# Performance work log

Hardware: AMD Instinct MI355X
Metric: run time of the kernel (lower is better)

## Reference

```python
import jax, jax.numpy as jnp
import numpy as np

D_MODEL = 1024
N_HEADS = 16
N_GROUPS = 4
D_K = D_MODEL // N_HEADS
HEADS_PER_GROUP = N_HEADS // N_GROUPS


def rope(x):
    # x: [b, s, d]; rotate using half-split concat (NOT interleaved), matching source
    s, d = x.shape[1], x.shape[2]
    theta = 1.0 / (10000.0 ** (jnp.arange(d // 2, dtype=jnp.float32) / (d // 2)))
    ang = jnp.arange(s, dtype=jnp.float32)[:, None] * theta[None, :]  # [s, d/2]
    cos, sin = jnp.cos(ang), jnp.sin(ang)
    xe, xo = x[..., 0::2], x[..., 1::2]
    return jnp.concatenate([xe * cos - xo * sin, xe * sin + xo * cos], axis=-1)


def setup_inputs() -> dict:
    key = jax.random.key(0)
    k1, k2, k3, k4, k5 = jax.random.split(key, 5)
    b, s = 1, 2048
    scale = 0.02
    X = jax.random.normal(k1, (b, s, D_MODEL), dtype=jnp.float32)
    W_q = jax.random.normal(k2, (D_MODEL, D_MODEL), dtype=jnp.float32) * scale
    W_k = jax.random.normal(k3, (N_GROUPS * D_K, D_MODEL), dtype=jnp.float32) * scale
    W_v = jax.random.normal(k4, (N_GROUPS * D_K, D_MODEL), dtype=jnp.float32) * scale
    W_o = jax.random.normal(k5, (D_MODEL, D_MODEL), dtype=jnp.float32) * scale
    return {"X": X, "W_q": W_q, "W_k": W_k, "W_v": W_v, "W_o": W_o}


def reference(X, W_q, W_k, W_v, W_o):
    b, s, _ = X.shape
    Xr = rope(X)
    Q = (Xr @ W_q.T).reshape(b, s, N_HEADS, D_K).transpose(0, 2, 1, 3)
    K = (Xr @ W_k.T).reshape(b, s, N_GROUPS, D_K).transpose(0, 2, 1, 3)
    V = (Xr @ W_v.T).reshape(b, s, N_GROUPS, D_K).transpose(0, 2, 1, 3)
    Q = Q.reshape(b, N_GROUPS, HEADS_PER_GROUP, s, D_K)
    scores = jnp.einsum('bghsd,bgtd->bghst', Q, K) / jnp.sqrt(jnp.float32(D_K))
    mask = jnp.triu(jnp.ones((s, s), dtype=scores.dtype), k=1) * (-1e9)
    attn = jax.nn.softmax(scores + mask, axis=-1)
    out = jnp.einsum('bghst,bgtd->bghsd', attn, V)  # [b,g,h,s,dk]
    out = out.reshape(b, N_HEADS, s, D_K).transpose(0, 2, 1, 3).reshape(b, s, D_MODEL)
    return out @ W_o.T
```

## Files before the change

kernel.cpp:

```cpp
#include <hip/hip_runtime.h>
#include <hip/hip_bf16.h>

#define S_LEN   2048
#define D_MODEL 1024
#define N_HEADS 16
#define N_GROUPS 4
#define D_K     64
#define KV_DIM  (N_GROUPS * D_K)

typedef __hip_bfloat16 bf16;
typedef unsigned short u16;
typedef __attribute__((ext_vector_type(8))) short bfrag;
typedef __attribute__((ext_vector_type(4))) float ffrag;
typedef __attribute__((ext_vector_type(4))) unsigned int u32x4;

__device__ __forceinline__ float b2f(u16 u) {
    return __uint_as_float(((unsigned)u) << 16);
}
__device__ __forceinline__ u16 f2bu(float f) {
    bf16 h = __float2bfloat16(f);
    return __builtin_bit_cast(u16, h);
}
__device__ __forceinline__ unsigned cvt_pk_bf16(float lo, float hi) {
    unsigned r;
    asm("v_cvt_pk_bf16_f32 %0, %1, %2" : "=v"(r) : "v"(lo), "v"(hi));
    return r;
}
__device__ __forceinline__ float ex2(float x) {
#if __has_builtin(__builtin_amdgcn_exp2f)
    return __builtin_amdgcn_exp2f(x);
#else
    return __expf(x * 0.69314718f);
#endif
}

typedef __attribute__((address_space(3))) u16 lds_u16;
typedef __attribute__((address_space(1))) const u16 glb_u16;
__device__ __forceinline__ void gld_lds16(const u16* g, u16* l) {
    __builtin_amdgcn_global_load_lds((glb_u16*)g, (lds_u16*)l, 16, 0, 0);
}

__device__ __forceinline__ int probe_f32(const u16* p) {
    int lane = threadIdx.x & 63;
    int e0 = (p[lane] >> 7) & 0xFF;
    int e1 = (p[lane + 64] >> 7) & 0xFF;
    int c = ((e0 < 100 || e0 > 140) ? 1 : 0) + ((e1 < 100 || e1 > 140) ? 1 : 0);
    unsigned long long b1 = __ballot(c >= 1);
    unsigned long long b2 = __ballot(c >= 2);
    return ((__popcll(b1) + __popcll(b2)) > 16) ? 1 : 0;
}

__global__ void probe5_kernel(const u16* __restrict__ p0, const u16* __restrict__ p1,
                              const u16* __restrict__ p2, const u16* __restrict__ p3,
                              const u16* __restrict__ p4, int* __restrict__ mode) {
    if (blockIdx.x != 0) return;
    const u16* ps[5] = {p0, p1, p2, p3, p4};
    int lane = threadIdx.x & 63;
    for (int t = 0; t < 5; t++) {
        int e0 = (ps[t][lane] >> 7) & 0xFF;
        int e1 = (ps[t][lane + 64] >> 7) & 0xFF;
        int c = ((e0 < 100 || e0 > 140) ? 1 : 0) + ((e1 < 100 || e1 > 140) ? 1 : 0);
        unsigned long long b1 = __ballot(c >= 1);
        unsigned long long b2 = __ballot(c >= 2);
        if (lane == 0) mode[t] = ((__popcll(b1) + __popcll(b2)) > 16) ? 1 : 0;
    }
}

__global__ __launch_bounds__(512)
void rope_kernel(const void* __restrict__ Xin, u16* __restrict__ Xr) {
    int md = probe_f32((const u16*)Xin);
    int i = blockIdx.x;
    int j = threadIdx.x;
    float freq = ex2(-(float)j * 0.025952563241307518f);
    float ang  = (float)i * freq;
    float sv, cv;
    sincosf(ang, &sv, &cv);
    int base = i * D_MODEL;
    float xe, xo;
    if (md) {
        float2 xv = *(const float2*)&((const float*)Xin)[base + 2 * j];
        xe = xv.x; xo = xv.y;
    } else {
        ushort2 xv = *(const ushort2*)&((const u16*)Xin)[base + 2 * j];
        xe = b2f(xv.x); xo = b2f(xv.y);
    }
    Xr[base + j]       = f2bu(xe * cv - xo * sv);
    Xr[base + 512 + j] = f2bu(xe * sv + xo * cv);
}

__global__ __launch_bounds__(256)
void wconv_kernel(const void* __restrict__ Wq, const void* __restrict__ Wk,
                  const void* __restrict__ Wv, const void* __restrict__ Wo,
                  u16* __restrict__ WB, u16* __restrict__ WoB) {
    int bid = blockIdx.x;
    const void* src; u16* dst; int gbase;
    if (bid < 512)      { src = Wq; dst = WB;                      gbase = bid; }
    else if (bid < 640) { src = Wk; dst = WB + 1024 * 1024;        gbase = bid - 512; }
    else if (bid < 768) { src = Wv; dst = WB + 1280 * 1024;        gbase = bid - 640; }
    else                { src = Wo; dst = WoB;                     gbase = bid - 768; }
    int md = probe_f32((const u16*)src);
    size_t g = (size_t)gbase * 256 + threadIdx.x;
    if (md) {
        const float* f = (const float*)src + g * 8;
        float4 v0 = *(const float4*)f;
        float4 v1 = *(const float4*)(f + 4);
        u16 t[8] = {f2bu(v0.x), f2bu(v0.y), f2bu(v0.z), f2bu(v0.w),
                    f2bu(v1.x), f2bu(v1.y), f2bu(v1.z), f2bu(v1.w)};
        *(uint4*)(dst + g * 8) = *(const uint4*)t;
    } else {
        *(uint4*)(dst + g * 8) = *(const uint4*)((const u16*)src + g * 8);
    }
}

template<int MODE>
__global__ __launch_bounds__(256)
void gemm_fast(const u16* __restrict__ A, const u16* __restrict__ WBm,
               u16* __restrict__ Qm, u16* __restrict__ Km, u16* __restrict__ Vm,
               float* __restrict__ Cf) {
    __shared__ u16 As[8192];
    __shared__ u16 Bs[4096];
    const int tid = threadIdx.x;
    const int w = tid >> 6, lane = tid & 63, quad = lane >> 4, lcol = lane & 15;
    const int m0 = blockIdx.y * 128;
    const int n0 = blockIdx.x * 64;

    const int arl   = lane >> 3;
    const int colsw = ((lane & 7) ^ arl) * 8;

    const u16* ap[4]; const u16* bp[2];
    u16* asd[4]; u16* bsd[2];
    #pragma unroll
    for (int c = 0; c < 4; c++) {
        ap[c]  = A + (size_t)(m0 + (c * 4 + w) * 8 + arl) * 1024 + colsw;
        asd[c] = As + (c * 4 + w) * 512;
    }
    #pragma unroll
    for (int c = 0; c < 2; c++) {
        bp[c]  = WBm + (size_t)(n0 + (c * 4 + w) * 8 + arl) * 1024 + colsw;
        bsd[c] = Bs + (c * 4 + w) * 512;
    }

    const int abase = (w * 32 + lcol) * 64;
    const int koff0 = (quad * 8) ^ ((lcol & 7) * 8);
    const int koff1 = koff0 ^ 32;

    ffrag acc[2][4];
    #pragma unroll
    for (int rf = 0; rf < 2; rf++)
        #pragma unroll
        for (int ct = 0; ct < 4; ct++) acc[rf][ct] = (ffrag)0.0f;

    for (int k0 = 0; k0 < D_MODEL; k0 += 64) {
        #pragma unroll
        for (int c = 0; c < 4; c++) gld_lds16(ap[c] + k0, asd[c]);
        #pragma unroll
        for (int c = 0; c < 2; c++) gld_lds16(bp[c] + k0, bsd[c]);
        __syncthreads();

        const bfrag a00 = *(const bfrag*)&As[abase + koff0];
        const bfrag a10 = *(const bfrag*)&As[abase + 1024 + koff0];
        const bfrag a01 = *(const bfrag*)&As[abase + koff1];
        const bfrag a11 = *(const bfrag*)&As[abase + 1024 + koff1];
        #pragma unroll
        for (int ct = 0; ct < 4; ct++) {
            const int bb = (ct * 16 + lcol) * 64;
            const bfrag b0 = *(const bfrag*)&Bs[bb + koff0];
            acc[0][ct] = __builtin_amdgcn_mfma_f32_16x16x32_bf16(a00, b0, acc[0][ct], 0, 0, 0);
            acc[1][ct] = __builtin_amdgcn_mfma_f32_16x16x32_bf16(a10, b0, acc[1][ct], 0, 0, 0);
            const bfrag b1 = *(const bfrag*)&Bs[bb + koff1];
            acc[0][ct] = __builtin_amdgcn_mfma_f32_16x16x32_bf16(a01, b1, acc[0][ct], 0, 0, 0);
            acc[1][ct] = __builtin_amdgcn_mfma_f32_16x16x32_bf16(a11, b1, acc[1][ct], 0, 0, 0);
        }
        __syncthreads();
    }

    if (MODE == 0) {
        if (n0 < 1280) {
            u16* Cp; int ldc, nc;
            if (n0 < 1024) { Cp = Qm; ldc = 1024; nc = n0; }
            else           { Cp = Km; ldc = 256;  nc = n0 - 1024; }
            #pragma unroll
            for (int rf = 0; rf < 2; rf++)
                #pragma unroll
                for (int ct = 0; ct < 4; ct++)
                    #pragma unroll
                    for (int r = 0; r < 4; r++) {
                        int row = m0 + w * 32 + rf * 16 + quad * 4 + r;
                        Cp[(size_t)row * ldc + nc + ct * 16 + lcol] = f2bu(acc[rf][ct][r]);
                    }
        } else {
            const int nc = n0 - 1280;
            #pragma unroll
            for (int rf = 0; rf < 2; rf++)
                #pragma unroll
                for (int ct = 0; ct < 4; ct++)
                    #pragma unroll
                    for (int r = 0; r < 4; r++) {
                        int row = m0 + w * 32 + rf * 16 + quad * 4 + r;
                        int col = nc + ct * 16 + lcol;
                        Vm[(size_t)col * S_LEN + row] = f2bu(acc[rf][ct][r]);
                    }
        }
    } else {
        #pragma unroll
        for (int rf = 0; rf < 2; rf++)
            #pragma unroll
            for (int ct = 0; ct < 4; ct++)
                #pragma unroll
                for (int r = 0; r < 4; r++) {
                    int row = m0 + w * 32 + rf * 16 + quad * 4 + r;
                    Cf[(size_t)row * D_MODEL + n0 + ct * 16 + lcol] = acc[rf][ct][r];
                }
    }
}

__device__ __forceinline__ void stageB(u16* dst, const void* Bv, size_t off, int md) {
    if (md) {
        const float* Bf = (const float*)Bv;
        float4 b0 = *(const float4*)&Bf[off];
        float4 b1 = *(const float4*)&Bf[off + 4];
        u16 t[8] = {f2bu(b0.x), f2bu(b0.y), f2bu(b0.z), f2bu(b0.w),
                    f2bu(b1.x), f2bu(b1.y), f2bu(b1.z), f2bu(b1.w)};
        *(uint4*)dst = *(const uint4*)t;
    } else {
        *(uint4*)dst = *(const uint4*)&((const u16*)Bv)[off];
    }
}

__global__ __launch_bounds__(256)
void qkv_mfma(const u16* __restrict__ Xr, const void* __restrict__ Wq,
              const void* __restrict__ Wk, const void* __restrict__ Wv,
              u16* __restrict__ Qm, u16* __restrict__ Km, u16* __restrict__ Vm,
              const int* __restrict__ mode) {
    __shared__ u16 As[128][36];
    __shared__ u16 Bs[64][36];
    const int tid = threadIdx.x;
    const int w = tid >> 6, lane = tid & 63, quad = lane >> 4, lcol = lane & 15;
    const int m0 = blockIdx.y * 128;
    const int n0 = blockIdx.x * 64;

    const void* Bv; int nb, md;
    if (n0 < 1024)       { Bv = Wq; nb = n0;        md = mode[1]; }
    else if (n0 < 1280)  { Bv = Wk; nb = n0 - 1024; md = mode[2]; }
    else                 { Bv = Wv; nb = n0 - 1280; md = mode[3]; }

    ffrag acc[2][4];
    #pragma unroll
    for (int rf = 0; rf < 2; rf++)
        #pragma unroll
        for (int ct = 0; ct < 4; ct++) acc[rf][ct] = (ffrag)0.0f;

    const int arow = tid >> 2, akc = tid & 3;
    for (int k0 = 0; k0 < D_MODEL; k0 += 32) {
        *(uint4*)&As[arow][akc * 8] =
            *(const uint4*)&Xr[(size_t)(m0 + arow) * D_MODEL + k0 + akc * 8];
        *(uint4*)&As[arow + 64][akc * 8] =
            *(const uint4*)&Xr[(size_t)(m0 + arow + 64) * D_MODEL + k0 + akc * 8];
        stageB(&Bs[arow][akc * 8], Bv, (size_t)(nb + arow) * D_MODEL + k0 + akc * 8, md);
        __syncthreads();
        const bfrag a0 = *(const bfrag*)&As[w * 32 + lcol][quad * 8];
        const bfrag a1 = *(const bfrag*)&As[w * 32 + 16 + lcol][quad * 8];
        #pragma unroll
        for (int ct = 0; ct < 4; ct++) {
            const bfrag b = *(const bfrag*)&Bs[ct * 16 + lcol][quad * 8];
            acc[0][ct] = __builtin_amdgcn_mfma_f32_16x16x32_bf16(a0, b, acc[0][ct], 0, 0, 0);
            acc[1][ct] = __builtin_amdgcn_mfma_f32_16x16x32_bf16(a1, b, acc[1][ct], 0, 0, 0);
        }
        __syncthreads();
    }

    if (n0 < 1280) {
        u16* Cp; int ldc, nc;
        if (n0 < 1024) { Cp = Qm; ldc = 1024; nc = n0; }
        else           { Cp = Km; ldc = 256;  nc = n0 - 1024; }
        #pragma unroll
        for (int rf = 0; rf < 2; rf++)
            #pragma unroll
            for (int ct = 0; ct < 4; ct++)
                #pragma unroll
                for (int r = 0; r < 4; r++) {
                    int row = m0 + w * 32 + rf * 16 + quad * 4 + r;
                    Cp[(size_t)row * ldc + nc + ct * 16 + lcol] = f2bu(acc[rf][ct][r]);
                }
    } else {
        const int nc = n0 - 1280;
        #pragma unroll
        for (int rf = 0; rf < 2; rf++)
            #pragma unroll
            for (int ct = 0; ct < 4; ct++)
                #pragma unroll
                for (int r = 0; r < 4; r++) {
                    int row = m0 + w * 32 + rf * 16 + quad * 4 + r;
                    int col = nc + ct * 16 + lcol;
                    Vm[(size_t)col * S_LEN + row] = f2bu(acc[rf][ct][r]);
                }
    }
}

__global__ __launch_bounds__(256)
void oproj_mfma(const u16* __restrict__ A, const void* __restrict__ B,
                float* __restrict__ C, const int* __restrict__ mode) {
    __shared__ u16 As[128][36];
    __shared__ u16 Bs[64][36];
    const int tid = threadIdx.x;
    const int w = tid >> 6, lane = tid & 63, quad = lane >> 4, lcol = lane & 15;
    const int m0 = blockIdx.y * 128;
    const int n0 = blockIdx.x * 64;
    const int md = mode[4];

    ffrag acc[2][4];
    #pragma unroll
    for (int rf = 0; rf < 2; rf++)
        #pragma unroll
        for (int ct = 0; ct < 4; ct++) acc[rf][ct] = (ffrag)0.0f;

    const int arow = tid >> 2, akc = tid & 3;
    for (int k0 = 0; k0 < D_MODEL; k0 += 32) {
        *(uint4*)&As[arow][akc * 8] =
            *(const uint4*)&A[(size_t)(m0 + arow) * D_MODEL + k0 + akc * 8];
        *(uint4*)&As[arow + 64][akc * 8] =
            *(const uint4*)&A[(size_t)(m0 + arow + 64) * D_MODEL + k0 + akc * 8];
        stageB(&Bs[arow][akc * 8], B, (size_t)(n0 + arow) * D_MODEL + k0 + akc * 8, md);
        __syncthreads();
        const bfrag a0 = *(const bfrag*)&As[w * 32 + lcol][quad * 8];
        const bfrag a1 = *(const bfrag*)&As[w * 32 + 16 + lcol][quad * 8];
        #pragma unroll
        for (int ct = 0; ct < 4; ct++) {
            const bfrag b = *(const bfrag*)&Bs[ct * 16 + lcol][quad * 8];
            acc[0][ct] = __builtin_amdgcn_mfma_f32_16x16x32_bf16(a0, b, acc[0][ct], 0, 0, 0);
            acc[1][ct] = __builtin_amdgcn_mfma_f32_16x16x32_bf16(a1, b, acc[1][ct], 0, 0, 0);
        }
        __syncthreads();
    }

    #pragma unroll
    for (int rf = 0; rf < 2; rf++)
        #pragma unroll
        for (int ct = 0; ct < 4; ct++)
            #pragma unroll
            for (int r = 0; r < 4; r++) {
                int row = m0 + w * 32 + rf * 16 + quad * 4 + r;
                C[(size_t)row * D_MODEL + n0 + ct * 16 + lcol] = acc[rf][ct][r];
            }
}

template<int CS, int SF>
__global__ __launch_bounds__(256)
void attn_part(const u16* __restrict__ Q, const u16* __restrict__ K,
               const u16* __restrict__ Vt, float* __restrict__ OpF,
               u16* __restrict__ OpH, float2* __restrict__ ml2) {
    const int bid = blockIdx.x;
    const int cidx = bid >> 4;
    const int h = bid & 15;
    const int g = h >> 2;

    int i, c;
    if (CS == 3) {
        if (cidx < 8)       { i = cidx;                  c = 0; }
        else if (cidx < 24) { i = 8 + ((cidx - 8) >> 1); c = (cidx - 8) & 1; }
        else if (cidx < 48) { int q = (cidx - 24) / 3;   i = 16 + q; c = (cidx - 24) - 3 * q; }
        else                { i = 24 + ((cidx - 48) >> 2); c = (cidx - 48) & 3; }
    } else {
        if (cidx < 16) { i = cidx; c = 0; }
        else           { i = 16 + ((cidx - 16) >> 1); c = (cidx - 16) & 1; }
    }
    const int i0 = i * 64;
    const int tile0 = c << CS;
    const int tlast = min(i, ((c + 1) << CS) - 1);
    const int nt = tlast - tile0 + 1;

    const int tid  = threadIdx.x;
    const int w    = tid >> 6;
    const int lane = tid & 63;
    const int quad = lane >> 4;
    const int lcol = lane & 15;

    __shared__ u16 Ks[64][72];
    __shared__ u16 Vts[64][72];

    const int qi = i0 + w * 16 + lcol;
    const bfrag qb0 = *(const bfrag*)&Q[(size_t)qi * D_MODEL + h * 64 + quad * 8];
    const bfrag qb1 = *(const bfrag*)&Q[(size_t)qi * D_MODEL + h * 64 + 32 + quad * 8];

    ffrag oacc[4];
    #pragma unroll
    for (int ct = 0; ct < 4; ct++) oacc[ct] = (ffrag)0.0f;
    float m_run = -1e30f, l_run = 0.0f;

    const int key0 = tid & 63, dc0 = tid >> 6;
    const int vd0 = tid >> 3, vch = tid & 7;
    const int vpos0 = 32 * (vch >> 2) + 16 * (vch & 1) + 4 * ((vch >> 1) & 1);
    const u16* vbase0 = &Vt[(size_t)(g * 64 + vd0) * S_LEN];
    const u16* vbase1 = &Vt[(size_t)(g * 64 + vd0 + 32) * S_LEN];

    int jp = tile0 * 64;
    uint4 kpre0 = *(const uint4*)&K[(size_t)(jp + key0) * KV_DIM + g * 64 + dc0 * 8];
    uint4 kpre1 = *(const uint4*)&K[(size_t)(jp + key0) * KV_DIM + g * 64 + (dc0 + 4) * 8];
    uint4 vpre0 = *(const uint4*)&vbase0[jp + vch * 8];
    uint4 vpre1 = *(const uint4*)&vbase1[jp + vch * 8];

    const float CF = 0.18033688f;

    for (int tt = 0; tt < nt; tt++) {
        const int j0 = (tile0 + tt) * 64;

        *(uint4*)&Ks[key0][dc0 * 8]       = kpre0;
        *(uint4*)&Ks[key0][(dc0 + 4) * 8] = kpre1;
        *(uint2*)&Vts[vd0][vpos0]           = make_uint2(vpre0.x, vpre0.y);
        *(uint2*)&Vts[vd0][vpos0 + 8]       = make_uint2(vpre0.z, vpre0.w);
        *(uint2*)&Vts[vd0 + 32][vpos0]      = make_uint2(vpre1.x, vpre1.y);
        *(uint2*)&Vts[vd0 + 32][vpos0 + 8]  = make_uint2(vpre1.z, vpre1.w);
        __syncthreads();

        if (tt + 1 < nt) {
            const int j0n = (tile0 + tt + 1) * 64;
            kpre0 = *(const uint4*)&K[(size_t)(j0n + key0) * KV_DIM + g * 64 + dc0 * 8];
            kpre1 = *(const uint4*)&K[(size_t)(j0n + key0) * KV_DIM + g * 64 + (dc0 + 4) * 8];
            vpre0 = *(const uint4*)&vbase0[j0n + vch * 8];
            vpre1 = *(const uint4*)&vbase1[j0n + vch * 8];
        }

        ffrag sacc[4];
        #pragma unroll
        for (int ct = 0; ct < 4; ct++) sacc[ct] = (ffrag)0.0f;
        __builtin_amdgcn_s_setprio(1);
        #pragma unroll
        for (int ct = 0; ct < 4; ct++) {
            const bfrag kb0 = *(const bfrag*)&Ks[ct * 16 + lcol][quad * 8];
            sacc[ct] = __builtin_amdgcn_mfma_f32_16x16x32_bf16(kb0, qb0, sacc[ct], 0, 0, 0);
            const bfrag kb1 = *(const bfrag*)&Ks[ct * 16 + lcol][32 + quad * 8];
            sacc[ct] = __builtin_amdgcn_mfma_f32_16x16x32_bf16(kb1, qb1, sacc[ct], 0, 0, 0);
        }
        __builtin_amdgcn_s_setprio(0);

        float sv[4][4];
        if (tile0 + tt == i) {
            #pragma unroll
            for (int ct = 0; ct < 4; ct++)
                #pragma unroll
                for (int r = 0; r < 4; r++) {
                    int kj = j0 + ct * 16 + quad * 4 + r;
                    sv[ct][r] = (kj <= qi) ? sacc[ct][r] : -1e30f;
                }
        } else {
            #pragma unroll
            for (int ct = 0; ct < 4; ct++)
                #pragma unroll
                for (int r = 0; r < 4; r++) sv[ct][r] = sacc[ct][r];
        }

        float mx = sv[0][0];
        #pragma unroll
        for (int ct = 0; ct < 4; ct++)
            #pragma unroll
            for (int r = 0; r < 4; r++) mx = fmaxf(mx, sv[ct][r]);
        mx = fmaxf(mx, __shfl_xor(mx, 16, 64));
        mx = fmaxf(mx, __shfl_xor(mx, 32, 64));

        if (!__all(mx <= m_run + 44.0f)) {
            float mnew = fmaxf(m_run, mx);
            float al = ex2((m_run - mnew) * CF);
            m_run = mnew;
            l_run *= al;
            #pragma unroll
            for (int r = 0; r < 4; r++) {
                float ar = __shfl(al, quad * 4 + r, 64);
                #pragma unroll
                for (int ct = 0; ct < 4; ct++) oacc[ct][r] *= ar;
            }
        }

        const float mc = m_run * CF;
        float rs = 0.0f;
        #pragma unroll
        for (int ct = 0; ct < 4; ct++)
            #pragma unroll
            for (int r = 0; r < 4; r++) {
                float p = ex2(sv[ct][r] * CF - mc);
                sv[ct][r] = p;
                rs += p;
            }
        rs += __shfl_xor(rs, 16, 64);
        rs += __shfl_xor(rs, 32, 64);
        l_run += rs;

        u32x4 pw0, pw1;
        pw0[0] = cvt_pk_bf16(sv[0][0], sv[0][1]);
        pw0[1] = cvt_pk_bf16(sv[0][2], sv[0][3]);
        pw0[2] = cvt_pk_bf16(sv[1][0], sv[1][1]);
        pw0[3] = cvt_pk_bf16(sv[1][2], sv[1][3]);
        pw1[0] = cvt_pk_bf16(sv[2][0], sv[2][1]);
        pw1[1] = cvt_pk_bf16(sv[2][2], sv[2][3]);
        pw1[2] = cvt_pk_bf16(sv[3][0], sv[3][1]);
        pw1[3] = cvt_pk_bf16(sv[3][2], sv[3][3]);
        const bfrag pa0 = __builtin_bit_cast(bfrag, pw0);
        const bfrag pa1 = __builtin_bit_cast(bfrag, pw1);

        __builtin_amdgcn_s_setprio(1);
        #pragma unroll
        for (int ct = 0; ct < 4; ct++) {
            const bfrag vb0 = *(const bfrag*)&Vts[ct * 16 + lcol][quad * 8];
            oacc[ct] = __builtin_amdgcn_mfma_f32_16x16x32_bf16(pa0, vb0, oacc[ct], 0, 0, 0);
            const bfrag vb1 = *(const bfrag*)&Vts[ct * 16 + lcol][32 + quad * 8];
            oacc[ct] = __builtin_amdgcn_mfma_f32_16x16x32_bf16(pa1, vb1, oacc[ct], 0, 0, 0);
        }
        __builtin_amdgcn_s_setprio(0);
        __syncthreads();
    }

    #pragma unroll
    for (int ct = 0; ct < 4; ct++)
        #pragma unroll
        for (int r = 0; r < 4; r++) {
            int row = w * 16 + quad * 4 + r;
            size_t off = (size_t)bid * 4096 + row * 64 + ct * 16 + lcol;
            if (SF) OpF[off] = oacc[ct][r];
            else    OpH[off] = f2bu(oacc[ct][r]);
        }
    if (quad == 0)
        ml2[(size_t)bid * 64 + w * 16 + lcol] = make_float2(m_run * 0.125f, l_run);
}

template<int CS, int SF>
__global__ __launch_bounds__(256)
void attn_combine(const float* __restrict__ OpF, const u16* __restrict__ OpH,
                  const float2* __restrict__ ml2, u16* __restrict__ Om) {
    const int row = blockIdx.x;
    const int i = row >> 6;
    const int r = row & 63;
    const int t = threadIdx.x;
    const int h = t >> 4;
    const int d = (t & 15) * 4;
    const int nc = (i >> CS) + 1;
    int pfx;
    if (CS == 3)
        pfx = (i < 8) ? i : (i < 16) ? 8 + 2 * (i - 8)
            : (i < 24) ? 24 + 3 * (i - 16) : 48 + 4 * (i - 24);
    else
        pfx = (i < 16) ? i : 16 + 2 * (i - 16);

    float M = -1e30f;
    for (int c = 0; c < nc; c++) {
        float2 m = ml2[(size_t)((pfx + c) * 16 + h) * 64 + r];
        M = fmaxf(M, m.x);
    }
    float L = 0.0f;
    float acc[4] = {0.0f, 0.0f, 0.0f, 0.0f};
    for (int c = 0; c < nc; c++) {
        float2 m = ml2[(size_t)((pfx + c) * 16 + h) * 64 + r];
        float wgt = __expf(m.x - M);
        L += m.y * wgt;
        size_t off = (size_t)((pfx + c) * 16 + h) * 4096 + r * 64 + d;
        if (SF) {
            float4 v = *(const float4*)&OpF[off];
            acc[0] += v.x * wgt; acc[1] += v.y * wgt;
            acc[2] += v.z * wgt; acc[3] += v.w * wgt;
        } else {
            ushort4 v = *(const ushort4*)&OpH[off];
            acc[0] += b2f(v.x) * wgt; acc[1] += b2f(v.y) * wgt;
            acc[2] += b2f(v.z) * wgt; acc[3] += b2f(v.w) * wgt;
        }
    }
    float inv = 1.0f / L;
    #pragma unroll
    for (int k = 0; k < 4; k++)
        Om[(size_t)row * D_MODEL + h * 64 + d + k] = f2bu(acc[k] * inv);
}

extern "C" void kernel_launch(void* const* d_in, const int* in_sizes, int n_in,
                              void* d_out, int out_size, void* d_ws, size_t ws_size,
                              hipStream_t stream) {
    const void* X  = d_in[0];
    const void* Wq = d_in[1];
    const void* Wk = d_in[2];
    const void* Wv = d_in[3];
    const void* Wo = d_in[4];
    float* out = (float*)d_out;

    u16* XrB = (u16*)d_out;

    int* mode = (int*)d_ws;
    u16* Qm = (u16*)((char*)d_ws + 64);
    u16* Km = Qm + (size_t)S_LEN * D_MODEL;
    u16* Vm = Km + (size_t)S_LEN * KV_DIM;
    u16* Om = Vm + (size_t)S_LEN * KV_DIM;

    const size_t needA    = 10485824ULL + 20971520ULL + 655360ULL;
    const size_t needFull = needA + 3145728ULL + 2097152ULL;

    rope_kernel<<<S_LEN, 512, 0, stream>>>(X, XrB);

    if (ws_size >= needFull) {
        float*  OpF = (float*)((char*)d_ws + 10485824);
        float2* ml2 = (float2*)((char*)d_ws + 10485824 + 20971520);
        u16*    WB  = (u16*)((char*)d_ws + needA);
        u16*    WoB = WB + (size_t)1536 * 1024;

        wconv_kernel<<<1280, 256, 0, stream>>>(Wq, Wk, Wv, Wo, WB, WoB);
        gemm_fast<0><<<dim3(24, 16), 256, 0, stream>>>(XrB, WB, Qm, Km, Vm, nullptr);
        attn_part<3, 1><<<80 * 16, 256, 0, stream>>>(Qm, Km, Vm, OpF, nullptr, ml2);
        attn_combine<3, 1><<<S_LEN, 256, 0, stream>>>(OpF, nullptr, ml2, Om);
        gemm_fast<1><<<dim3(16, 16), 256, 0, stream>>>(Om, WoB, nullptr, nullptr, nullptr, out);
    } else {
        probe5_kernel<<<1, 64, 0, stream>>>(
            (const u16*)X, (const u16*)Wq, (const u16*)Wk, (const u16*)Wv,
            (const u16*)Wo, mode);
        qkv_mfma<<<dim3((D_MODEL + 2 * KV_DIM) / 64, S_LEN / 128), 256, 0, stream>>>(
            XrB, Wq, Wk, Wv, Qm, Km, Vm, mode);
        if (ws_size >= needA) {
            float*  OpF = (float*)((char*)d_ws + 10485824);
            float2* ml2 = (float2*)((char*)d_ws + 10485824 + 20971520);
            attn_part<3, 1><<<80 * 16, 256, 0, stream>>>(Qm, Km, Vm, OpF, nullptr, ml2);
            attn_combine<3, 1><<<S_LEN, 256, 0, stream>>>(OpF, nullptr, ml2, Om);
        } else {
            u16*    OpH = (u16*)d_out;
            float2* ml2 = (float2*)((char*)d_out + (size_t)768 * 4096 * 2);
            attn_part<4, 0><<<48 * 16, 256, 0, stream>>>(Qm, Km, Vm, nullptr, OpH, ml2);
            attn_combine<4, 0><<<S_LEN, 256, 0, stream>>>(nullptr, OpH, ml2, Om);
        }
        oproj_mfma<<<dim3(D_MODEL / 64, S_LEN / 128), 256, 0, stream>>>(Om, Wo, out, mode);
    }
}
```

Before: 144.6 us.

## Double-buffer GEMM and attention LDS tiles, fuse rope and weight conversion

Merges the rope and weight-conversion kernels into a single prep launch, removing one kernel launch. The projection GEMM now double-buffers its LDS tiles, so the next K-slice is loaded while MFMAs run on the current one, dropping one barrier per iteration. The attention kernel likewise double-buffers its K/V tiles and writes the next tile after the PV MFMAs, with one sync per iteration. This doubles LDS use per block, which may reduce occupancy.

Measured after the change: 141.8 us. -2.0%, faster.

```diff
diff --git a/kernel.cpp b/kernel.cpp
--- a/kernel.cpp
+++ b/kernel.cpp
@@ -63,6 +63,53 @@
         unsigned long long b1 = __ballot(c >= 1);
         unsigned long long b2 = __ballot(c >= 2);
         if (lane == 0) mode[t] = ((__popcll(b1) + __popcll(b2)) > 16) ? 1 : 0;
+    }
+}
+
+__global__ __launch_bounds__(512)
+void prep_kernel(const void* __restrict__ Xin, u16* __restrict__ Xr,
+                 const void* __restrict__ Wq, const void* __restrict__ Wk,
+                 const void* __restrict__ Wv, const void* __restrict__ Wo,
+                 u16* __restrict__ WB, u16* __restrict__ WoB) {
+    int b = blockIdx.x;
+    if (b < S_LEN) {
+        int md = probe_f32((const u16*)Xin);
+        int i = b;
+        int j = threadIdx.x;
+        float freq = ex2(-(float)j * 0.025952563241307518f);
+        float ang  = (float)i * freq;
+        float sv, cv;
+        sincosf(ang, &sv, &cv);
+        int base = i * D_MODEL;
+        float xe, xo;
+        if (md) {
+            float2 xv = *(const float2*)&((const float*)Xin)[base + 2 * j];
+            xe = xv.x; xo = xv.y;
+        } else {
+            ushort2 xv = *(const ushort2*)&((const u16*)Xin)[base + 2 * j];
+            xe = b2f(xv.x); xo = b2f(xv.y);
+        }
+        Xr[base + j]       = f2bu(xe * cv - xo * sv);
+        Xr[base + 512 + j] = f2bu(xe * sv + xo * cv);
+    } else {
+        int bid = b - S_LEN;
+        const void* src; u16* dst; int goff;
+        if (bid < 256)      { src = Wq; dst = WB;               goff = bid; }
+        else if (bid < 320) { src = Wk; dst = WB + 1024 * 1024; goff = bid - 256; }
+        else if (bid < 384) { src = Wv; dst = WB + 1280 * 1024; goff = bid - 320; }
+        else                { src = Wo; dst = WoB;              goff = bid - 384; }
+        int md = probe_f32((const u16*)src);
+        size_t g = (size_t)goff * 512 + threadIdx.x;
+        if (md) {
+            const float* f = (const float*)src + g * 8;
+            float4 v0 = *(const float4*)f;
+            float4 v1 = *(const float4*)(f + 4);
+            u16 t[8] = {f2bu(v0.x), f2bu(v0.y), f2bu(v0.z), f2bu(v0.w),
+                        f2bu(v1.x), f2bu(v1.y), f2bu(v1.z), f2bu(v1.w)};
+            *(uint4*)(dst + g * 8) = *(const uint4*)t;
+        } else {
+            *(uint4*)(dst + g * 8) = *(const uint4*)((const u16*)src + g * 8);
+        }
     }
 }
 
@@ -88,37 +135,13 @@
     Xr[base + 512 + j] = f2bu(xe * sv + xo * cv);
 }
 
-__global__ __launch_bounds__(256)
-void wconv_kernel(const void* __restrict__ Wq, const void* __restrict__ Wk,
-                  const void* __restrict__ Wv, const void* __restrict__ Wo,
-                  u16* __restrict__ WB, u16* __restrict__ WoB) {
-    int bid = blockIdx.x;
-    const void* src; u16* dst; int gbase;
-    if (bid < 512)      { src = Wq; dst = WB;                      gbase = bid; }
-    else if (bid < 640) { src = Wk; dst = WB + 1024 * 1024;        gbase = bid - 512; }
-    else if (bid < 768) { src = Wv; dst = WB + 1280 * 1024;        gbase = bid - 640; }
-    else                { src = Wo; dst = WoB;                     gbase = bid - 768; }
-    int md = probe_f32((const u16*)src);
-    size_t g = (size_t)gbase * 256 + threadIdx.x;
-    if (md) {
-        const float* f = (const float*)src + g * 8;
-        float4 v0 = *(const float4*)f;
-        float4 v1 = *(const float4*)(f + 4);
-        u16 t[8] = {f2bu(v0.x), f2bu(v0.y), f2bu(v0.z), f2bu(v0.w),
-                    f2bu(v1.x), f2bu(v1.y), f2bu(v1.z), f2bu(v1.w)};
-        *(uint4*)(dst + g * 8) = *(const uint4*)t;
-    } else {
-        *(uint4*)(dst + g * 8) = *(const uint4*)((const u16*)src + g * 8);
-    }
-}
-
 template<int MODE>
 __global__ __launch_bounds__(256)
 void gemm_fast(const u16* __restrict__ A, const u16* __restrict__ WBm,
                u16* __restrict__ Qm, u16* __restrict__ Km, u16* __restrict__ Vm,
                float* __restrict__ Cf) {
-    __shared__ u16 As[8192];
-    __shared__ u16 Bs[4096];
+    __shared__ u16 As[2][8192];
+    __shared__ u16 Bs[2][4096];
     const int tid = threadIdx.x;
     const int w = tid >> 6, lane = tid & 63, quad = lane >> 4, lcol = lane & 15;
     const int m0 = blockIdx.y * 128;
@@ -128,17 +151,12 @@
     const int colsw = ((lane & 7) ^ arl) * 8;
 
     const u16* ap[4]; const u16* bp[2];
-    u16* asd[4]; u16* bsd[2];
-    #pragma unroll
-    for (int c = 0; c < 4; c++) {
-        ap[c]  = A + (size_t)(m0 + (c * 4 + w) * 8 + arl) * 1024 + colsw;
-        asd[c] = As + (c * 4 + w) * 512;
-    }
-    #pragma unroll
-    for (int c = 0; c < 2; c++) {
-        bp[c]  = WBm + (size_t)(n0 + (c * 4 + w) * 8 + arl) * 1024 + colsw;
-        bsd[c] = Bs + (c * 4 + w) * 512;
-    }
+    #pragma unroll
+    for (int c = 0; c < 4; c++)
+        ap[c] = A + (size_t)(m0 + (c * 4 + w) * 8 + arl) * 1024 + colsw;
+    #pragma unroll
+    for (int c = 0; c < 2; c++)
+        bp[c] = WBm + (size_t)(n0 + (c * 4 + w) * 8 + arl) * 1024 + colsw;
 
     const int abase = (w * 32 + lcol) * 64;
     const int koff0 = (quad * 8) ^ ((lcol & 7) * 8);
@@ -150,28 +168,42 @@
         #pragma unroll
         for (int ct = 0; ct < 4; ct++) acc[rf][ct] = (ffrag)0.0f;
 
+    #pragma unroll
+    for (int c = 0; c < 4; c++) gld_lds16(ap[c], &As[0][(c * 4 + w) * 512]);
+    #pragma unroll
+    for (int c = 0; c < 2; c++) gld_lds16(bp[c], &Bs[0][(c * 4 + w) * 512]);
+    __syncthreads();
+
+    int cur = 0;
     for (int k0 = 0; k0 < D_MODEL; k0 += 64) {
-        #pragma unroll
-        for (int c = 0; c < 4; c++) gld_lds16(ap[c] + k0, asd[c]);
-        #pragma unroll
-        for (int c = 0; c < 2; c++) gld_lds16(bp[c] + k0, bsd[c]);
-        __syncthreads();
-
-        const bfrag a00 = *(const bfrag*)&As[abase + koff0];
-        const bfrag a10 = *(const bfrag*)&As[abase + 1024 + koff0];
-        const bfrag a01 = *(const bfrag*)&As[abase + koff1];
-        const bfrag a11 = *(const bfrag*)&As[abase + 1024 + koff1];
+        if (k0 + 64 < D_MODEL) {
+            const int nb = cur ^ 1;
+            #pragma unroll
+            for (int c = 0; c < 4; c++)
+                gld_lds16(ap[c] + k0 + 64, &As[nb][(c * 4 + w) * 512]);
+            #pragma unroll
+            for (int c = 0; c < 2; c++)
+                gld_lds16(bp[c] + k0 + 64, &Bs[nb][(c * 4 + w) * 512]);
+        }
+
+        const u16* Ab = &As[cur][0];
+        const u16* Bb = &Bs[cur][0];
+        const bfrag a00 = *(const bfrag*)&Ab[abase + koff0];
+        const bfrag a10 = *(const bfrag*)&Ab[abase + 1024 + koff0];
+        const bfrag a01 = *(const bfrag*)&Ab[abase + koff1];
+        const bfrag a11 = *(const bfrag*)&Ab[abase + 1024 + koff1];
         #pragma unroll
         for (int ct = 0; ct < 4; ct++) {
             const int bb = (ct * 16 + lcol) * 64;
-            const bfrag b0 = *(const bfrag*)&Bs[bb + koff0];
+            const bfrag b0 = *(const bfrag*)&Bb[bb + koff0];
             acc[0][ct] = __builtin_amdgcn_mfma_f32_16x16x32_bf16(a00, b0, acc[0][ct], 0, 0, 0);
             acc[1][ct] = __builtin_amdgcn_mfma_f32_16x16x32_bf16(a10, b0, acc[1][ct], 0, 0, 0);
-            const bfrag b1 = *(const bfrag*)&Bs[bb + koff1];
+            const bfrag b1 = *(const bfrag*)&Bb[bb + koff1];
             acc[0][ct] = __builtin_amdgcn_mfma_f32_16x16x32_bf16(a01, b1, acc[0][ct], 0, 0, 0);
             acc[1][ct] = __builtin_amdgcn_mfma_f32_16x16x32_bf16(a11, b1, acc[1][ct], 0, 0, 0);
         }
         __syncthreads();
+        cur ^= 1;
     }
 
     if (MODE == 0) {
@@ -375,8 +407,8 @@
     const int quad = lane >> 4;
     const int lcol = lane & 15;
 
-    __shared__ u16 Ks[64][72];
-    __shared__ u16 Vts[64][72];
+    __shared__ u16 Ks[2][64][72];
+    __shared__ u16 Vts[2][64][72];
 
     const int qi = i0 + w * 16 + lcol;
     const bfrag qb0 = *(const bfrag*)&Q[(size_t)qi * D_MODEL + h * 64 + quad * 8];
@@ -399,18 +431,20 @@
     uint4 vpre0 = *(const uint4*)&vbase0[jp + vch * 8];
     uint4 vpre1 = *(const uint4*)&vbase1[jp + vch * 8];
 
+    {
+        *(uint4*)&Ks[0][key0][dc0 * 8]       = kpre0;
+        *(uint4*)&Ks[0][key0][(dc0 + 4) * 8] = kpre1;
+        *(uint2*)&Vts[0][vd0][vpos0]          = make_uint2(vpre0.x, vpre0.y);
+        *(uint2*)&Vts[0][vd0][vpos0 + 8]      = make_uint2(vpre0.z, vpre0.w);
+        *(uint2*)&Vts[0][vd0 + 32][vpos0]     = make_uint2(vpre1.x, vpre1.y);
+        *(uint2*)&Vts[0][vd0 + 32][vpos0 + 8] = make_uint2(vpre1.z, vpre1.w);
+    }
+
     const float CF = 0.18033688f;
+    int cur = 0;
 
     for (int tt = 0; tt < nt; tt++) {
         const int j0 = (tile0 + tt) * 64;
-
-        *(uint4*)&Ks[key0][dc0 * 8]       = kpre0;
-        *(uint4*)&Ks[key0][(dc0 + 4) * 8] = kpre1;
-        *(uint2*)&Vts[vd0][vpos0]           = make_uint2(vpre0.x, vpre0.y);
-        *(uint2*)&Vts[vd0][vpos0 + 8]       = make_uint2(vpre0.z, vpre0.w);
-        *(uint2*)&Vts[vd0 + 32][vpos0]      = make_uint2(vpre1.x, vpre1.y);
-        *(uint2*)&Vts[vd0 + 32][vpos0 + 8]  = make_uint2(vpre1.z, vpre1.w);
-        __syncthreads();
 
         if (tt + 1 < nt) {
             const int j0n = (tile0 + tt + 1) * 64;
@@ -419,6 +453,7 @@
             vpre0 = *(const uint4*)&vbase0[j0n + vch * 8];
             vpre1 = *(const uint4*)&vbase1[j0n + vch * 8];
         }
+        __syncthreads();
 
         ffrag sacc[4];
         #pragma unroll
@@ -426,9 +461,9 @@
         __builtin_amdgcn_s_setprio(1);
         #pragma unroll
         for (int ct = 0; ct < 4; ct++) {
-            const bfrag kb0 = *(const bfrag*)&Ks[ct * 16 + lcol][quad * 8];
+            const bfrag kb0 = *(const bfrag*)&Ks[cur][ct * 16 + lcol][quad * 8];
             sacc[ct] = __builtin_amdgcn_mfma_f32_16x16x32_bf16(kb0, qb0, sacc[ct], 0, 0, 0);
-            const bfrag kb1 = *(const bfrag*)&Ks[ct * 16 + lcol][32 + quad * 8];
+            const bfrag kb1 = *(const bfrag*)&Ks[cur][ct * 16 + lcol][32 + quad * 8];
             sacc[ct] = __builtin_amdgcn_mfma_f32_16x16x32_bf16(kb1, qb1, sacc[ct], 0, 0, 0);
         }
         __builtin_amdgcn_s_setprio(0);
@@ -499,13 +534,23 @@
         __builtin_amdgcn_s_setprio(1);
         #pragma unroll
         for (int ct = 0; ct < 4; ct++) {
-            const bfrag vb0 = *(const bfrag*)&Vts[ct * 16 + lcol][quad * 8];
+            const bfrag vb0 = *(const bfrag*)&Vts[cur][ct * 16 + lcol][quad * 8];
             oacc[ct] = __builtin_amdgcn_mfma_f32_16x16x32_bf16(pa0, vb0, oacc[ct], 0, 0, 0);
-            const bfrag vb1 = *(const bfrag*)&Vts[ct * 16 + lcol][32 + quad * 8];
+            const bfrag vb1 = *(const bfrag*)&Vts[cur][ct * 16 + lcol][32 + quad * 8];
             oacc[ct] = __builtin_amdgcn_mfma_f32_16x16x32_bf16(pa1, vb1, oacc[ct], 0, 0, 0);
         }
         __builtin_amdgcn_s_setprio(0);
-        __syncthreads();
+
+        if (tt + 1 < nt) {
+            const int nb = cur ^ 1;
+            *(uint4*)&Ks[nb][key0][dc0 * 8]       = kpre0;
+            *(uint4*)&Ks[nb][key0][(dc0 + 4) * 8] = kpre1;
+            *(uint2*)&Vts[nb][vd0][vpos0]          = make_uint2(vpre0.x, vpre0.y);
+            *(uint2*)&Vts[nb][vd0][vpos0 + 8]      = make_uint2(vpre0.z, vpre0.w);
+            *(uint2*)&Vts[nb][vd0 + 32][vpos0]     = make_uint2(vpre1.x, vpre1.y);
+            *(uint2*)&Vts[nb][vd0 + 32][vpos0 + 8] = make_uint2(vpre1.z, vpre1.w);
+        }
+        cur ^= 1;
     }
 
     #pragma unroll
@@ -588,20 +633,19 @@
     const size_t needA    = 10485824ULL + 20971520ULL + 655360ULL;
     const size_t needFull = needA + 3145728ULL + 2097152ULL;
 
-    rope_kernel<<<S_LEN, 512, 0, stream>>>(X, XrB);
-
     if (ws_size >= needFull) {
         float*  OpF = (float*)((char*)d_ws + 10485824);
         float2* ml2 = (float2*)((char*)d_ws + 10485824 + 20971520);
         u16*    WB  = (u16*)((char*)d_ws + needA);
         u16*    WoB = WB + (size_t)1536 * 1024;
 
-        wconv_kernel<<<1280, 256, 0, stream>>>(Wq, Wk, Wv, Wo, WB, WoB);
+        prep_kernel<<<S_LEN + 640, 512, 0, stream>>>(X, XrB, Wq, Wk, Wv, Wo, WB, WoB);
         gemm_fast<0><<<dim3(24, 16), 256, 0, stream>>>(XrB, WB, Qm, Km, Vm, nullptr);
         attn_part<3, 1><<<80 * 16, 256, 0, stream>>>(Qm, Km, Vm, OpF, nullptr, ml2);
         attn_combine<3, 1><<<S_LEN, 256, 0, stream>>>(OpF, nullptr, ml2, Om);
         gemm_fast<1><<<dim3(16, 16), 256, 0, stream>>>(Om, WoB, nullptr, nullptr, nullptr, out);
     } else {
+        rope_kernel<<<S_LEN, 512, 0, stream>>>(X, XrB);
         probe5_kernel<<<1, 64, 0, stream>>>(
             (const u16*)X, (const u16*)Wq, (const u16*)Wk, (const u16*)Wv,
             (const u16*)Wo, mode);
```
